# Kernel optimization log

Measured on AMD Instinct MI355X. Metric: run time of the kernel, lower is better.

The kernel has to match this reference:

```python
import jax, jax.numpy as jnp
import numpy as np

B, N, K = 4, 2048, 48
NUM_RBF = 16
NUM_PE = 16
MAX_REL = 32
EDGE_C = 128
PE_IN = 2 * MAX_REL + 2  # 66


def setup_inputs() -> dict:
    key = jax.random.key(0)
    ks = jax.random.split(key, 10)
    coords = jax.random.normal(ks[0], (B, N, 3), dtype=jnp.float32) * 10.0
    token_exists_mask = jnp.ones((B, N), dtype=jnp.float32)
    token_bonds = (jax.random.uniform(ks[1], (B, N, N)) < 0.01).astype(jnp.float32)
    pe_w = jax.random.normal(ks[2], (PE_IN, NUM_PE), dtype=jnp.float32) * 0.05
    pe_b = jnp.zeros((NUM_PE,), dtype=jnp.float32)
    edge_w = jax.random.normal(ks[3], (NUM_PE + NUM_RBF + 1, EDGE_C), dtype=jnp.float32) * 0.05
    ln_g = jnp.ones((EDGE_C,), dtype=jnp.float32)
    ln_b = jnp.zeros((EDGE_C,), dtype=jnp.float32)
    token_to_center_atom = jax.random.randint(ks[4], (B, N), 0, N, dtype=jnp.int32)
    residue_index = jnp.sort(jax.random.randint(ks[5], (B, N), 0, 4096, dtype=jnp.int32), axis=-1)
    asym_id = jax.random.randint(ks[6], (B, N), 0, 4, dtype=jnp.int32)
    is_ligand = jax.random.randint(ks[7], (B, N), 0, 2, dtype=jnp.int32)
    return {
        'coords': coords, 'token_exists_mask': token_exists_mask,
        'token_bonds': token_bonds, 'pe_w': pe_w, 'pe_b': pe_b,
        'edge_w': edge_w, 'ln_g': ln_g, 'ln_b': ln_b,
        'token_to_center_atom': token_to_center_atom,
        'residue_index': residue_index, 'asym_id': asym_id,
        'is_ligand': is_ligand,
    }


def _gather_edges(M, E_idx):
    # M: [B, N, N], E_idx: [B, N, K] -> [B, N, K]
    return jnp.take_along_axis(M, E_idx, axis=2)


def _rbf(D):
    # D: [..., K] -> [..., K, NUM_RBF]
    D_mu = jnp.linspace(2.0, 22.0, NUM_RBF)
    D_sigma = (22.0 - 2.0) / NUM_RBF
    return jnp.exp(-(((D[..., None] - D_mu) / D_sigma) ** 2))


def reference(coords, token_exists_mask, token_bonds, pe_w, pe_b, edge_w,
              ln_g, ln_b, token_to_center_atom, residue_index, asym_id, is_ligand):
    # token coords: center atom per token, masked
    X = jnp.take_along_axis(coords, token_to_center_atom[..., None], axis=1)
    X = X * token_exists_mask[..., None]  # [B, N, 3]

    # masked pairwise distances + KNN (smallest K, sorted ascending)
    mask = token_exists_mask
    mask_2d = mask[:, None, :] * mask[:, :, None]  # [B, N, N]
    dX = X[:, :, None, :] - X[:, None, :, :]
    D = mask_2d * jnp.sqrt(jnp.sum(dX * dX, axis=-1) + 1e-6)
    D_max = jnp.max(D, axis=-1, keepdims=True)
    D_adjust = D + (1.0 - mask_2d) * D_max
    neg_D, E_idx = jax.lax.top_k(-D_adjust, K)  # largest of -D == smallest of D
    D_neighbors = -neg_D  # [B, N, K]

    RBF_all = _rbf(D_neighbors)  # [B, N, K, NUM_RBF]

    # relative sequence position features
    offset = residue_index[:, :, None] - residue_index[:, None, :]  # [B, N, N]
    offset_e = _gather_edges(offset, E_idx)  # [B, N, K]
    chain_labels = jnp.zeros_like(asym_id)  # use_multichain_encoding=False
    d_chains = (chain_labels[:, :, None] - chain_labels[:, None, :] == 0).astype(jnp.int32)
    E_chains = _gather_edges(d_chains, E_idx)  # [B, N, K]
    d = jnp.clip(offset_e + MAX_REL, 0, 2 * MAX_REL) * E_chains + (1 - E_chains) * (2 * MAX_REL + 1)
    d_onehot = jax.nn.one_hot(d, PE_IN, dtype=jnp.float32)
    E_positional = d_onehot @ pe_w + pe_b  # [B, N, K, NUM_PE]

    # ligand-gated bond feature
    lig = is_ligand.astype(bool)
    tb_mask = (lig[:, :, None] | lig[:, None, :]).astype(token_bonds.dtype)
    tb = token_bonds * tb_mask
    tb_e = _gather_edges(tb, E_idx)[..., None]  # [B, N, K, 1]

    # fuse, embed, layernorm
    E = jnp.concatenate([E_positional, RBF_all, tb_e], axis=-1)  # [B, N, K, 33]
    E = E @ edge_w  # [B, N, K, EDGE_C]
    mu = jnp.mean(E, axis=-1, keepdims=True)
    var = jnp.mean((E - mu) ** 2, axis=-1, keepdims=True)
    E = (E - mu) / jnp.sqrt(var + 1e-5) * ln_g + ln_b
    return (E, E_idx, D_neighbors)
```

## Files before the change

kernel.cpp:

```cpp
#include <hip/hip_runtime.h>
#include <math.h>

namespace {
constexpr int B_ = 4;
constexpr int N_ = 2048;
constexpr int K_ = 48;
constexpr int MAX_REL_ = 32;
constexpr int EDGE_C_ = 128;
constexpr int NUM_PE_ = 16;
constexpr int NROWS = B_ * N_;
constexpr int NEDGE = NROWS * K_;
}

__global__ __launch_bounds__(256) void x_kernel(const float* __restrict__ coords,
                                                const float* __restrict__ mask,
                                                const int* __restrict__ t2ca,
                                                float4* __restrict__ X4) {
    int r = blockIdx.x * 256 + threadIdx.x;
    if (r >= NROWS) return;
    int b = r >> 11;
    int c = t2ca[r];
    float m = mask[r];
    const float* s = coords + ((size_t)(b * N_ + c)) * 3;
    X4[r] = make_float4(__fmul_rn(s[0], m), __fmul_rn(s[1], m),
                        __fmul_rn(s[2], m), m);
}

__global__ __launch_bounds__(256) void prep_kernel(const float* __restrict__ pe_w,
                                                   const float* __restrict__ pe_b,
                                                   const float* __restrict__ edge_w,
                                                   const float* __restrict__ ln_g,
                                                   float* __restrict__ Wg,
                                                   float* __restrict__ C1g,
                                                   float* __restrict__ T12_2,
                                                   float* __restrict__ A22,
                                                   float* __restrict__ A23_2,
                                                   float* __restrict__ V0,
                                                   float* __restrict__ Tb1_2,
                                                   float* __restrict__ A33) {
    __shared__ float sW[33][129];
    __shared__ float sC[65][129];
    __shared__ float sm[33];
    const int tid = threadIdx.x;
    const int wv = tid >> 6;
    const int lane = tid & 63;

    for (int idx = tid; idx < 33 * 128; idx += 256)
        sW[idx >> 7][idx & 127] = edge_w[idx];
    __syncthreads();
    for (int r = wv; r < 33; r += 4) {
        float v = sW[r][lane] + sW[r][64 + lane];
        #pragma unroll
        for (int off = 32; off; off >>= 1) v += __shfl_xor(v, off, 64);
        if (lane == 0) sm[r] = v * (1.0f / 128.0f);
    }
    __syncthreads();
    for (int idx = tid; idx < 33 * 128; idx += 256) {
        int p = idx >> 7, c = idx & 127;
        float cen = sW[p][c] - sm[p];
        sW[p][c] = cen;
        if (p >= 16) Wg[(p - 16) * 128 + c] = cen * ln_g[c];
    }
    __syncthreads();
    for (int idx = tid; idx < 65 * 128; idx += 256) {
        int d = idx >> 7, c = idx & 127;
        float acc = 0.0f;
        #pragma unroll
        for (int q = 0; q < 16; ++q)
            acc = fmaf(pe_w[d * 16 + q] + pe_b[q], sW[q][c], acc);
        sC[d][c] = acc;
        C1g[idx] = acc * ln_g[c];
    }
    __syncthreads();
    for (int idx = tid; idx < 1443; idx += 256) {
        const float* u; const float* v; float scale; float* dst;
        if (idx < 1040) {
            int d = idx >> 4, r = idx & 15;
            u = &sC[d][0]; v = &sW[16 + r][0];
            scale = 2.0f / 128.0f; dst = T12_2 + idx;
        } else if (idx < 1105) {
            int d = idx - 1040;
            u = &sC[d][0]; v = u; scale = 1.0f / 128.0f; dst = V0 + d;
        } else if (idx < 1170) {
            int d = idx - 1105;
            u = &sC[d][0]; v = &sW[32][0]; scale = 2.0f / 128.0f; dst = Tb1_2 + d;
        } else if (idx < 1426) {
            int i = idx - 1170; int r = i >> 4, s = i & 15;
            u = &sW[16 + r][0]; v = &sW[16 + s][0];
            scale = 1.0f / 128.0f; dst = A22 + i;
        } else if (idx < 1442) {
            int r = idx - 1426;
            u = &sW[16 + r][0]; v = &sW[32][0];
            scale = 2.0f / 128.0f; dst = A23_2 + r;
        } else {
            u = &sW[32][0]; v = u; scale = 1.0f / 128.0f; dst = A33;
        }
        float a = 0.0f;
        #pragma unroll 8
        for (int c = 0; c < 128; ++c) a = fmaf(u[c], v[c], a);
        *dst = a * scale;
    }
}

__global__ __launch_bounds__(256) void knn_kernel(const float4* __restrict__ X4,
                                                  float* __restrict__ eidx_f,
                                                  float* __restrict__ dneb) {
    __shared__ unsigned s_hist[4][256];
    __shared__ unsigned long long s_cbuf[4][64];
    const int wv = threadIdx.x >> 6;
    const int lane = threadIdx.x & 63;
    const int row = blockIdx.x * 4 + wv;
    const int b = row >> 11;

    const float4 xi = X4[row];
    const float mi = xi.w;
    const float4* Xb = X4 + (size_t)b * N_;

    unsigned fb[32];
    unsigned mz = 0u;
    float lmax = -INFINITY;
    #pragma unroll
    for (int t = 0; t < 32; ++t) {
        const int j = t * 64 + lane;
        const float4 p = Xb[j];
        float dx = __fsub_rn(xi.x, p.x);
        float dy = __fsub_rn(xi.y, p.y);
        float dz = __fsub_rn(xi.z, p.z);
        float d2 = __fmaf_rn(dz, dz, __fmaf_rn(dx, dx, __fmul_rn(dy, dy)));
        float m2 = __fmul_rn(mi, p.w);
        float dd = __fmul_rn(m2, __fsqrt_rn(__fadd_rn(d2, 1e-6f)));
        fb[t] = __float_as_uint(dd);
        if (m2 == 0.0f) mz |= (1u << t);
        lmax = fmaxf(lmax, dd);
    }
    #pragma unroll
    for (int off = 32; off; off >>= 1) lmax = fmaxf(lmax, __shfl_xor(lmax, off, 64));

    unsigned fmin_l = 0xFFFFFFFFu, fmax_l = 0u;
    #pragma unroll
    for (int t = 0; t < 32; ++t) {
        float adj = ((mz >> t) & 1u) ? lmax : __uint_as_float(fb[t]);
        unsigned u = __float_as_uint(adj);
        fb[t] = u;
        fmin_l = min(fmin_l, u);
        fmax_l = max(fmax_l, u);
    }
    #pragma unroll
    for (int off = 32; off; off >>= 1) {
        fmin_l = min(fmin_l, (unsigned)__shfl_xor((int)fmin_l, off, 64));
        fmax_l = max(fmax_l, (unsigned)__shfl_xor((int)fmax_l, off, 64));
    }
    const unsigned fminb = fmin_l;
    const unsigned range = fmax_l - fminb;
    const int vbits = (range == 0u) ? 0 : (32 - __clz((int)range));
    const int L = vbits + 11;
    int sh = (L > 8) ? (L - 8) : 0;

    unsigned cand = 0xFFFFFFFFu;
    int k_rem = K_;
    unsigned long long T = 0ull;

    while (true) {
        s_hist[wv][4 * lane + 0] = 0u;
        s_hist[wv][4 * lane + 1] = 0u;
        s_hist[wv][4 * lane + 2] = 0u;
        s_hist[wv][4 * lane + 3] = 0u;
        __asm__ volatile("s_waitcnt lgkmcnt(0)" ::: "memory");
        #pragma unroll
        for (int t = 0; t < 32; ++t) {
            if ((cand >> t) & 1u) {
                unsigned dig;
                if (sh >= 11) {
                    dig = ((fb[t] - fminb) >> (sh - 11)) & 255u;
                } else {
                    unsigned long long key =
                        ((unsigned long long)(fb[t] - fminb) << 11)
                        | (unsigned long long)(unsigned)(t * 64 + lane);
                    dig = (unsigned)(key >> sh) & 255u;
                }
                atomicAdd(&s_hist[wv][dig], 1u);
            }
        }
        __asm__ volatile("s_waitcnt lgkmcnt(0)" ::: "memory");
        const unsigned c0 = s_hist[wv][4 * lane + 0];
        const unsigned c1 = s_hist[wv][4 * lane + 1];
        const unsigned c2 = s_hist[wv][4 * lane + 2];
        const unsigned c3 = s_hist[wv][4 * lane + 3];
        const unsigned s4 = c0 + c1 + c2 + c3;
        unsigned inc = s4;
        #pragma unroll
        for (int off = 1; off < 64; off <<= 1) {
            unsigned o = (unsigned)__shfl_up((int)inc, off, 64);
            if (lane >= off) inc += o;
        }
        const unsigned ex = inc - s4;
        const unsigned e1 = ex + c0, e2 = e1 + c1, e3 = e2 + c2;
        const unsigned kr = (unsigned)k_rem;
        int digl = -1; unsigned below = 0u, bc = 0u;
        if (ex < kr && kr <= e1)           { digl = 4 * lane + 0; below = ex; bc = c0; }
        else if (e1 < kr && kr <= e2)      { digl = 4 * lane + 1; below = e1; bc = c1; }
        else if (e2 < kr && kr <= e3)      { digl = 4 * lane + 2; below = e2; bc = c2; }
        else if (e3 < kr && kr <= e3 + c3) { digl = 4 * lane + 3; below = e3; bc = c3; }

        unsigned long long bal = __ballot(digl >= 0);
        int src = __ffsll((long long)bal) - 1;
        const int dstar = __shfl(digl, src, 64);
        below = (unsigned)__shfl((int)below, src, 64);
        bc    = (unsigned)__shfl((int)bc, src, 64);
        k_rem -= (int)below;

        unsigned nc = 0u;
        unsigned long long myT = 0ull;
        #pragma unroll
        for (int t = 0; t < 32; ++t) {
            if ((cand >> t) & 1u) {
                unsigned long long key =
                    ((unsigned long long)(fb[t] - fminb) << 11)
                    | (unsigned long long)(unsigned)(t * 64 + lane);
                unsigned dig;
                if (sh >= 11) dig = ((fb[t] - fminb) >> (sh - 11)) & 255u;
                else          dig = (unsigned)(key >> sh) & 255u;
                if (dig == (unsigned)dstar) { nc |= (1u << t); myT = key; }
            }
        }
        cand = nc;
        if (bc == 1u || sh == 0) {
            unsigned long long b2 = __ballot(cand != 0u);
            int owner = __ffsll((long long)b2) - 1;
            T = __shfl(myT, owner, 64);
            break;
        }
        sh = (sh > 8) ? (sh - 8) : 0;
    }

    const unsigned Tv = (unsigned)(T >> 11);
    const unsigned Tj = (unsigned)(T & 2047u);
    unsigned selm = 0u; int scnt = 0;
    #pragma unroll
    for (int t = 0; t < 32; ++t) {
        unsigned v = fb[t] - fminb;
        unsigned j = (unsigned)(t * 64 + lane);
        if (v < Tv || (v == Tv && j <= Tj)) { selm |= (1u << t); ++scnt; }
    }
    int isc = scnt;
    #pragma unroll
    for (int off = 1; off < 64; off <<= 1) {
        int o = __shfl_up(isc, off, 64);
        if (lane >= off) isc += o;
    }
    int pos = isc - scnt;
    #pragma unroll
    for (int t = 0; t < 32; ++t) {
        if ((selm >> t) & 1u) {
            s_cbuf[wv][pos] = ((unsigned long long)(fb[t] - fminb) << 11)
                            | (unsigned long long)(unsigned)(t * 64 + lane);
            ++pos;
        }
    }
    __asm__ volatile("s_waitcnt lgkmcnt(0)" ::: "memory");
    unsigned long long kk = (lane < K_) ? s_cbuf[wv][lane] : ~0ull;

    #pragma unroll
    for (int k2 = 2; k2 <= 64; k2 <<= 1) {
        #pragma unroll
        for (int j = k2 >> 1; j > 0; j >>= 1) {
            unsigned long long o = __shfl_xor(kk, j, 64);
            const bool dirAsc = ((lane & k2) == 0);
            const bool lower = ((lane & j) == 0);
            unsigned long long mn = (kk < o) ? kk : o;
            unsigned long long mx = (kk < o) ? o : kk;
            kk = (lower == dirAsc) ? mn : mx;
        }
    }

    if (lane < K_) {
        unsigned fbits = (unsigned)(kk >> 11) + fminb;
        unsigned ji = (unsigned)(kk & 2047u);
        dneb[(size_t)row * K_ + lane] = __uint_as_float(fbits);
        eidx_f[(size_t)row * K_ + lane] = (float)ji;
    }
}

__global__ __launch_bounds__(256, 4) void edge_kernel(const float* __restrict__ eidx_f,
                                                      const float* __restrict__ dneb,
                                                      const float* __restrict__ token_bonds,
                                                      const float* __restrict__ C1g,
                                                      const float* __restrict__ Wg,
                                                      const float* __restrict__ V0,
                                                      const float* __restrict__ T12_2,
                                                      const float* __restrict__ Tb1_2,
                                                      const float* __restrict__ A22,
                                                      const float* __restrict__ A23_2,
                                                      const float* __restrict__ A33,
                                                      const float* __restrict__ ln_b,
                                                      const int* __restrict__ res_idx,
                                                      const int* __restrict__ is_lig,
                                                      float* __restrict__ Eout) {
    __shared__ float s_rbf[4][K_][20];
    __shared__ float4 s_meta[4][K_];
    __shared__ float s_D[4][K_];
    const int tid = threadIdx.x;
    const int wv = tid >> 6;
    const int lane = tid & 63;
    const int row = blockIdx.x * 4 + wv;
    const int b = row >> 11;

    float w0[17], w1[17];
    #pragma unroll
    for (int p = 0; p < 17; ++p) {
        float2 w = ((const float2*)Wg)[p * 64 + lane];
        w0[p] = w.x; w1[p] = w.y;
    }
    const float bb0 = ln_b[2 * lane], bb1 = ln_b[2 * lane + 1];

    const int ri = res_idx[row];
    const int li = is_lig[row];

    int doff_l = 0; float tb_l = 0.0f;
    if (lane < K_) {
        const int e = row * K_ + lane;
        const int j = (int)(eidx_f[e] + 0.5f);
        const float D = dneb[e];
        const int jrow = b * N_ + j;
        const int rj = res_idx[jrow];
        const int lj = is_lig[jrow];
        float tb = token_bonds[(size_t)row * N_ + j];
        tb_l = (li | lj) ? tb : 0.0f;
        doff_l = min(max(ri - rj + MAX_REL_, 0), 2 * MAX_REL_);
        s_D[wv][lane] = D;
    }
    __syncthreads();

    #pragma unroll
    for (int t = 0; t < (K_ * NUM_PE_) / 64; ++t) {
        const int idx = t * 64 + lane;
        const int k = idx >> 4, r = idx & 15;
        const float D = s_D[wv][k];
        const float mu = 2.0f + (float)r * (4.0f / 3.0f);
        const float x = (D - mu) * 0.8f;
        s_rbf[wv][k][r] = __expf(-x * x);
    }
    __syncthreads();

    if (lane < K_) {
        float rr[16];
        const float* rb = &s_rbf[wv][lane][0];
        *(float4*)&rr[0]  = *(const float4*)&rb[0];
        *(float4*)&rr[4]  = *(const float4*)&rb[4];
        *(float4*)&rr[8]  = *(const float4*)&rb[8];
        *(float4*)&rr[12] = *(const float4*)&rb[12];
        float var = V0[doff_l];
        const float4* t12 = (const float4*)(T12_2 + doff_l * 16);
        float4 q0 = t12[0], q1 = t12[1], q2 = t12[2], q3 = t12[3];
        var = fmaf(rr[0], q0.x, var);  var = fmaf(rr[1], q0.y, var);
        var = fmaf(rr[2], q0.z, var);  var = fmaf(rr[3], q0.w, var);
        var = fmaf(rr[4], q1.x, var);  var = fmaf(rr[5], q1.y, var);
        var = fmaf(rr[6], q1.z, var);  var = fmaf(rr[7], q1.w, var);
        var = fmaf(rr[8], q2.x, var);  var = fmaf(rr[9], q2.y, var);
        var = fmaf(rr[10], q2.z, var); var = fmaf(rr[11], q2.w, var);
        var = fmaf(rr[12], q3.x, var); var = fmaf(rr[13], q3.y, var);
        var = fmaf(rr[14], q3.z, var); var = fmaf(rr[15], q3.w, var);
        #pragma unroll
        for (int r = 0; r < 16; ++r) {
            const float4* arow = (const float4*)(A22 + r * 16);
            float tr = 0.0f;
            #pragma unroll
            for (int s4 = 0; s4 < 4; ++s4) {
                float4 a = arow[s4];
                tr = fmaf(rr[s4 * 4 + 0], a.x, tr);
                tr = fmaf(rr[s4 * 4 + 1], a.y, tr);
                tr = fmaf(rr[s4 * 4 + 2], a.z, tr);
                tr = fmaf(rr[s4 * 4 + 3], a.w, tr);
            }
            var = fmaf(rr[r], tr, var);
        }
        if (tb_l != 0.0f) {
            float extra = Tb1_2[doff_l];
            #pragma unroll
            for (int r = 0; r < 16; ++r) extra = fmaf(rr[r], A23_2[r], extra);
            var = fmaf(tb_l, extra, var);
            var = fmaf(tb_l * tb_l, A33[0], var);
        }
        const float rstd = rsqrtf(var + 1e-5f);
        s_meta[wv][lane] = make_float4((float)doff_l, tb_l, rstd, 0.0f);
    }
    __syncthreads();

    unsigned long long* outp =
        (unsigned long long*)Eout + (size_t)row * K_ * 64 + lane;
    #pragma unroll 4
    for (int k = 0; k < K_; ++k) {
        const float4 mt = s_meta[wv][k];
        const int doffk = (int)mt.x;
        const float tbk = mt.y;
        const float rstd = mt.z;
        const float2 c1 = *(const float2*)(C1g + ((size_t)doffk << 7) + 2 * lane);

        float rr[16];
        const float* rb = &s_rbf[wv][k][0];
        *(float4*)&rr[0]  = *(const float4*)&rb[0];
        *(float4*)&rr[4]  = *(const float4*)&rb[4];
        *(float4*)&rr[8]  = *(const float4*)&rb[8];
        *(float4*)&rr[12] = *(const float4*)&rb[12];

        float ax = c1.x, ay = c1.y;
        #pragma unroll
        for (int p = 0; p < 16; ++p) {
            ax = fmaf(rr[p], w0[p], ax);
            ay = fmaf(rr[p], w1[p], ay);
        }
        if (tbk != 0.0f) {
            ax = fmaf(tbk, w0[16], ax);
            ay = fmaf(tbk, w1[16], ay);
        }
        union { float2 f; unsigned long long u; } cv;
        cv.f = make_float2(fmaf(ax, rstd, bb0), fmaf(ay, rstd, bb1));
        __builtin_nontemporal_store(cv.u, outp + (size_t)k * 64);
    }
}

extern "C" void kernel_launch(void* const* d_in, const int* in_sizes, int n_in,
                              void* d_out, int out_size, void* d_ws, size_t ws_size,
                              hipStream_t stream) {
    const float* coords      = (const float*)d_in[0];
    const float* mask        = (const float*)d_in[1];
    const float* token_bonds = (const float*)d_in[2];
    const float* pe_w        = (const float*)d_in[3];
    const float* pe_b        = (const float*)d_in[4];
    const float* edge_w      = (const float*)d_in[5];
    const float* ln_g        = (const float*)d_in[6];
    const float* ln_b        = (const float*)d_in[7];
    const int*   t2ca        = (const int*)d_in[8];
    const int*   res_idx     = (const int*)d_in[9];
    const int*   is_lig      = (const int*)d_in[11];

    float* out    = (float*)d_out;
    float* Eout   = out;
    float* eidx_f = out + (size_t)NEDGE * EDGE_C_;
    float* dneb   = eidx_f + NEDGE;

    float4* X4  = (float4*)d_ws;
    float* Wg   = (float*)d_ws + (size_t)NROWS * 4;
    float* C1g  = Wg + 17 * 128;
    float* T12  = C1g + 65 * 128;
    float* A22  = T12 + 1040;
    float* A23  = A22 + 256;
    float* V0   = A23 + 16;
    float* Tb1  = V0 + 65;
    float* A33  = Tb1 + 65;

    hipLaunchKernelGGL(x_kernel, dim3(NROWS / 256), dim3(256), 0, stream,
                       coords, mask, t2ca, X4);
    hipLaunchKernelGGL(prep_kernel, dim3(1), dim3(256), 0, stream,
                       pe_w, pe_b, edge_w, ln_g, Wg, C1g, T12, A22, A23, V0, Tb1, A33);
    hipLaunchKernelGGL(knn_kernel, dim3(NROWS / 4), dim3(256), 0, stream,
                       X4, eidx_f, dneb);
    hipLaunchKernelGGL(edge_kernel, dim3(NROWS / 4), dim3(256), 0, stream,
                       eidx_f, dneb, token_bonds, C1g, Wg, V0, T12, Tb1,
                       A22, A23, A33, ln_b, res_idx, is_lig, Eout);
}
```

Before: 428.1 us.

## Split single-block weight prep into three parallel kernels and cap KNN registers

The single-workgroup prep kernel, which computed the centered weights, the positional-encoding products and about 1443 dot products serially in one block, is split into three launches. The first centers the weights, the second uses 65 blocks for the C1 products and the third uses 6 blocks for the Gram-style dot products, with intermediates stored in the workspace instead of LDS. The KNN kernel also gets a launch-bounds occupancy hint of 6 and a partial unroll of its distance loop, which may reduce register pressure but can spill or slow the histogram selection. The split adds two extra kernel launches and global round trips for the intermediates.

```diff
diff --git a/kernel.cpp b/kernel.cpp
--- a/kernel.cpp
+++ b/kernel.cpp
@@ -26,85 +26,83 @@
                         __fmul_rn(s[2], m), m);
 }
 
-__global__ __launch_bounds__(256) void prep_kernel(const float* __restrict__ pe_w,
-                                                   const float* __restrict__ pe_b,
-                                                   const float* __restrict__ edge_w,
-                                                   const float* __restrict__ ln_g,
-                                                   float* __restrict__ Wg,
-                                                   float* __restrict__ C1g,
-                                                   float* __restrict__ T12_2,
-                                                   float* __restrict__ A22,
-                                                   float* __restrict__ A23_2,
-                                                   float* __restrict__ V0,
-                                                   float* __restrict__ Tb1_2,
-                                                   float* __restrict__ A33) {
-    __shared__ float sW[33][129];
-    __shared__ float sC[65][129];
+__global__ __launch_bounds__(256) void prep_a(const float* __restrict__ edge_w,
+                                              const float* __restrict__ ln_g,
+                                              float* __restrict__ Wcf,
+                                              float* __restrict__ Wg) {
     __shared__ float sm[33];
-    const int tid = threadIdx.x;
-    const int wv = tid >> 6;
-    const int lane = tid & 63;
-
-    for (int idx = tid; idx < 33 * 128; idx += 256)
-        sW[idx >> 7][idx & 127] = edge_w[idx];
-    __syncthreads();
+    const int wv = threadIdx.x >> 6;
+    const int lane = threadIdx.x & 63;
     for (int r = wv; r < 33; r += 4) {
-        float v = sW[r][lane] + sW[r][64 + lane];
+        float v = edge_w[r * 128 + lane] + edge_w[r * 128 + 64 + lane];
         #pragma unroll
         for (int off = 32; off; off >>= 1) v += __shfl_xor(v, off, 64);
         if (lane == 0) sm[r] = v * (1.0f / 128.0f);
     }
     __syncthreads();
-    for (int idx = tid; idx < 33 * 128; idx += 256) {
+    for (int idx = threadIdx.x; idx < 33 * 128; idx += 256) {
         int p = idx >> 7, c = idx & 127;
-        float cen = sW[p][c] - sm[p];
-        sW[p][c] = cen;
+        float cen = edge_w[idx] - sm[p];
+        Wcf[idx] = cen;
         if (p >= 16) Wg[(p - 16) * 128 + c] = cen * ln_g[c];
     }
-    __syncthreads();
-    for (int idx = tid; idx < 65 * 128; idx += 256) {
-        int d = idx >> 7, c = idx & 127;
-        float acc = 0.0f;
-        #pragma unroll
-        for (int q = 0; q < 16; ++q)
-            acc = fmaf(pe_w[d * 16 + q] + pe_b[q], sW[q][c], acc);
-        sC[d][c] = acc;
-        C1g[idx] = acc * ln_g[c];
-    }
-    __syncthreads();
-    for (int idx = tid; idx < 1443; idx += 256) {
-        const float* u; const float* v; float scale; float* dst;
-        if (idx < 1040) {
-            int d = idx >> 4, r = idx & 15;
-            u = &sC[d][0]; v = &sW[16 + r][0];
-            scale = 2.0f / 128.0f; dst = T12_2 + idx;
-        } else if (idx < 1105) {
-            int d = idx - 1040;
-            u = &sC[d][0]; v = u; scale = 1.0f / 128.0f; dst = V0 + d;
-        } else if (idx < 1170) {
-            int d = idx - 1105;
-            u = &sC[d][0]; v = &sW[32][0]; scale = 2.0f / 128.0f; dst = Tb1_2 + d;
-        } else if (idx < 1426) {
-            int i = idx - 1170; int r = i >> 4, s = i & 15;
-            u = &sW[16 + r][0]; v = &sW[16 + s][0];
-            scale = 1.0f / 128.0f; dst = A22 + i;
-        } else if (idx < 1442) {
-            int r = idx - 1426;
-            u = &sW[16 + r][0]; v = &sW[32][0];
-            scale = 2.0f / 128.0f; dst = A23_2 + r;
-        } else {
-            u = &sW[32][0]; v = u; scale = 1.0f / 128.0f; dst = A33;
-        }
-        float a = 0.0f;
-        #pragma unroll 8
-        for (int c = 0; c < 128; ++c) a = fmaf(u[c], v[c], a);
-        *dst = a * scale;
-    }
-}
-
-__global__ __launch_bounds__(256) void knn_kernel(const float4* __restrict__ X4,
-                                                  float* __restrict__ eidx_f,
-                                                  float* __restrict__ dneb) {
+}
+
+__global__ __launch_bounds__(128) void prep_b(const float* __restrict__ pe_w,
+                                              const float* __restrict__ pe_b,
+                                              const float* __restrict__ Wcf,
+                                              const float* __restrict__ ln_g,
+                                              float* __restrict__ C1c,
+                                              float* __restrict__ C1g) {
+    const int d = blockIdx.x, c = threadIdx.x;
+    float acc = 0.0f;
+    #pragma unroll
+    for (int q = 0; q < 16; ++q)
+        acc = fmaf(pe_w[d * 16 + q] + pe_b[q], Wcf[q * 128 + c], acc);
+    C1c[d * 128 + c] = acc;
+    C1g[d * 128 + c] = acc * ln_g[c];
+}
+
+__global__ __launch_bounds__(256) void prep_c(const float* __restrict__ Wcf,
+                                              const float* __restrict__ C1c,
+                                              float* __restrict__ V0,
+                                              float* __restrict__ T12_2,
+                                              float* __restrict__ Tb1_2,
+                                              float* __restrict__ A22,
+                                              float* __restrict__ A23_2,
+                                              float* __restrict__ A33) {
+    const int idx = blockIdx.x * 256 + threadIdx.x;
+    const float* u; const float* v; float scale; float* dst;
+    if (idx < 1040) {
+        int d = idx >> 4, r = idx & 15;
+        u = C1c + d * 128; v = Wcf + (16 + r) * 128;
+        scale = 2.0f / 128.0f; dst = T12_2 + idx;
+    } else if (idx < 1105) {
+        int d = idx - 1040;
+        u = C1c + d * 128; v = u; scale = 1.0f / 128.0f; dst = V0 + d;
+    } else if (idx < 1170) {
+        int d = idx - 1105;
+        u = C1c + d * 128; v = Wcf + 32 * 128; scale = 2.0f / 128.0f; dst = Tb1_2 + d;
+    } else if (idx < 1426) {
+        int i = idx - 1170; int r = i >> 4, s = i & 15;
+        u = Wcf + (16 + r) * 128; v = Wcf + (16 + s) * 128;
+        scale = 1.0f / 128.0f; dst = A22 + i;
+    } else if (idx < 1442) {
+        int r = idx - 1426;
+        u = Wcf + (16 + r) * 128; v = Wcf + 32 * 128;
+        scale = 2.0f / 128.0f; dst = A23_2 + r;
+    } else if (idx == 1442) {
+        u = Wcf + 32 * 128; v = u; scale = 1.0f / 128.0f; dst = A33;
+    } else return;
+    float a = 0.0f;
+    #pragma unroll 8
+    for (int c = 0; c < 128; ++c) a = fmaf(u[c], v[c], a);
+    *dst = a * scale;
+}
+
+__global__ __launch_bounds__(256, 6) void knn_kernel(const float4* __restrict__ X4,
+                                                     float* __restrict__ eidx_f,
+                                                     float* __restrict__ dneb) {
     __shared__ unsigned s_hist[4][256];
     __shared__ unsigned long long s_cbuf[4][64];
     const int wv = threadIdx.x >> 6;
@@ -119,7 +117,7 @@
     unsigned fb[32];
     unsigned mz = 0u;
     float lmax = -INFINITY;
-    #pragma unroll
+    #pragma unroll 4
     for (int t = 0; t < 32; ++t) {
         const int j = t * 64 + lane;
         const float4 p = Xb[j];
@@ -440,8 +438,10 @@
     float* dneb   = eidx_f + NEDGE;
 
     float4* X4  = (float4*)d_ws;
-    float* Wg   = (float*)d_ws + (size_t)NROWS * 4;
-    float* C1g  = Wg + 17 * 128;
+    float* Wcf  = (float*)d_ws + (size_t)NROWS * 4;
+    float* Wg   = Wcf + 33 * 128;
+    float* C1c  = Wg + 17 * 128;
+    float* C1g  = C1c + 65 * 128;
     float* T12  = C1g + 65 * 128;
     float* A22  = T12 + 1040;
     float* A23  = A22 + 256;
@@ -451,8 +451,12 @@
 
     hipLaunchKernelGGL(x_kernel, dim3(NROWS / 256), dim3(256), 0, stream,
                        coords, mask, t2ca, X4);
-    hipLaunchKernelGGL(prep_kernel, dim3(1), dim3(256), 0, stream,
-                       pe_w, pe_b, edge_w, ln_g, Wg, C1g, T12, A22, A23, V0, Tb1, A33);
+    hipLaunchKernelGGL(prep_a, dim3(1), dim3(256), 0, stream,
+                       edge_w, ln_g, Wcf, Wg);
+    hipLaunchKernelGGL(prep_b, dim3(65), dim3(128), 0, stream,
+                       pe_w, pe_b, Wcf, ln_g, C1c, C1g);
+    hipLaunchKernelGGL(prep_c, dim3(6), dim3(256), 0, stream,
+                       Wcf, C1c, V0, T12, Tb1, A22, A23, A33);
     hipLaunchKernelGGL(knn_kernel, dim3(NROWS / 4), dim3(256), 0, stream,
                        X4, eidx_f, dneb);
     hipLaunchKernelGGL(edge_kernel, dim3(NROWS / 4), dim3(256), 0, stream,
```

After: 787.0 us. 83.9% more time.
